# Performance work log

Measured on AMD Instinct MI355X. Metric: run time of the kernel, lower is better.

The kernel has to match this reference:

```python
import jax, jax.numpy as jnp
import numpy as np


def conv1d(x, w, b, pad):
    # x: [B,C,T], w: [O,I,K]
    y = jax.lax.conv_general_dilated(x, w, (1,), [(pad, pad)],
                                     dimension_numbers=('NCH', 'OIH', 'NCH'))
    return y + b[None, :, None]


def setup_inputs() -> dict:
    key = jax.random.key(0)
    ks = jax.random.split(key, 16)
    s = 0.05
    return {
        'x':    jax.random.normal(ks[0], (1024, 512), dtype=jnp.float32),
        'w1':   jax.random.normal(ks[1], (5, 1, 3), dtype=jnp.float32) * s,
        'b1':   jnp.zeros((5,), jnp.float32),
        'w2':   jax.random.normal(ks[2], (10, 5, 5), dtype=jnp.float32) * s,
        'b2':   jnp.zeros((10,), jnp.float32),
        'w3':   jax.random.normal(ks[3], (10, 10, 7), dtype=jnp.float32) * s,
        'b3':   jnp.zeros((10,), jnp.float32),
        'code': jax.random.uniform(ks[4], (10, 32), dtype=jnp.float32),
        'd1w':  jax.random.normal(ks[5], (10, 10, 5), dtype=jnp.float32) * s,
        'd1b':  jnp.zeros((10,), jnp.float32),
        'd2w':  jax.random.normal(ks[6], (10, 10, 5), dtype=jnp.float32) * s,
        'd2b':  jnp.zeros((10,), jnp.float32),
        'fcw':  jax.random.normal(ks[7], (512, 5120), dtype=jnp.float32) * 0.01,
        'fcb':  jnp.zeros((512,), jnp.float32),
    }


def reference(x, w1, b1, w2, b2, w3, b3, code, d1w, d1b, d2w, d2b, fcw, fcb):
    B = x.shape[0]
    h = x[:, None, :]                                   # [B,1,512]
    h = jax.nn.relu(conv1d(h, w1, b1, 1))               # [B,5,512]
    h = jax.nn.relu(conv1d(h, w2, b2, 2))               # [B,10,512]
    h = jnp.tanh(conv1d(h, w3, b3, 3))                  # [B,10,512]
    # squared distance: sum_c (h[b,c,t] - code[c,k])^2 -> [B,512,32]
    x2 = jnp.sum(h * h, axis=1)                         # [B,512]
    cross = jnp.einsum('bct,ck->btk', h, code)          # [B,512,32]
    c2 = jnp.sum(code * code, axis=0)                   # [32]
    dist = x2[:, :, None] - 2.0 * cross + c2[None, None, :]
    prob = jax.nn.softmax(-dist, axis=-1)               # [B,512,32]
    q = jnp.einsum('btk,ck->btc', prob, code)           # [B,512,10]
    h = q.transpose(0, 2, 1)                            # [B,10,512]
    h = jax.nn.relu(conv1d(h, d1w, d1b, 2))
    h = jax.nn.relu(conv1d(h, d2w, d2b, 2))
    flat = h.reshape(B, -1)                             # [B,5120]
    return jnp.tanh(flat @ fcw.T + fcb)                 # [B,512]
```

## Files before the change

### kernel.cpp

```cpp
#include <hip/hip_runtime.h>
#include <hip/hip_bf16.h>

#define TT 512
#define RS 16
#define RH 8
#define NROW 528
#define K_FC 5120

typedef _Float16 h8 __attribute__((ext_vector_type(8)));
typedef float f32x16 __attribute__((ext_vector_type(16)));
typedef __attribute__((address_space(1))) const void GAS;
typedef __attribute__((address_space(3))) void LAS;

__device__ __forceinline__ float fast_tanh(float v) {
    float e = __expf(2.0f * v);
    return 1.0f - 2.0f / (e + 1.0f);
}
__device__ __forceinline__ unsigned pk(float a, float b) {
    return __builtin_bit_cast(unsigned, __builtin_amdgcn_cvt_pkrtz(a, b));
}

__global__ __launch_bounds__(256) void prep_wtab_kernel(
    const float* __restrict__ w2, const float* __restrict__ w3,
    const float* __restrict__ d1w, const float* __restrict__ d2w,
    const float* __restrict__ code, uint4* __restrict__ wtab,
    unsigned* __restrict__ c2tab)
{
    const int i = blockIdx.x * 256 + threadIdx.x;
    if (i < 1600) {
        const int lane = i & 63;
        const int o = lane & 31;
        const int hi = lane >> 5;
        h8 v = {};
        if (i < 320) {
            const int j = i >> 6;
            #pragma unroll
            for (int e = 0; e < 8; ++e) {
                int k = hi * 8 + e;
                if (o < 10 && k < 5) v[e] = (_Float16)w2[(o * 5 + k) * 5 + j];
            }
        } else if (i < 768) {
            const int j = (i - 320) >> 6;
            #pragma unroll
            for (int e = 0; e < 8; ++e) {
                int k = hi * 8 + e;
                if (o < 10 && k < 10) v[e] = (_Float16)w3[(o * 10 + k) * 7 + j];
            }
        } else if (i < 1088) {
            const int j = (i - 768) >> 6;
            #pragma unroll
            for (int e = 0; e < 8; ++e) {
                int k = hi * 8 + e;
                if (o < 10 && k < 10) v[e] = (_Float16)d1w[(o * 10 + k) * 5 + j];
            }
        } else if (i < 1408) {
            const int j = (i - 1088) >> 6;
            #pragma unroll
            for (int e = 0; e < 8; ++e) {
                int k = hi * 8 + e;
                if (o < 10 && k < 10) v[e] = (_Float16)d2w[(o * 10 + k) * 5 + j];
            }
        } else if (i < 1472) {
            #pragma unroll
            for (int e = 0; e < 8; ++e) {
                int ch = hi * 8 + e;
                if (ch < 10) v[e] = (_Float16)(2.0f * code[ch * 32 + o]);
            }
        } else {
            const int ks = (i - 1472) >> 6;
            #pragma unroll
            for (int e = 0; e < 8; ++e) {
                int kc = ks * 16 + hi * 8 + e;
                if (o < 10) v[e] = (_Float16)code[o * 32 + kc];
            }
        }
        wtab[i] = __builtin_bit_cast(uint4, v);
    } else if (i < 1632) {
        int k = i - 1600;
        float s = 0.f;
        for (int c = 0; c < 10; ++c) { float cv = code[c * 32 + k]; s = fmaf(cv, cv, s); }
        c2tab[k] = __float_as_uint(4.0f - s);
    }
}

template<int J, int P, int ACT>
__device__ __forceinline__ void conv_stage(
    const _Float16* __restrict__ src, _Float16* __restrict__ dst,
    const uint4* __restrict__ wtab, int wbase, const float* __restrict__ bsrc)
{
    const int tid = threadIdx.x;
    const int lane = tid & 63;
    const int wv = tid >> 6;
    const int l31 = lane & 31;
    const int hi = lane >> 5;

    uint4 wf[J];
    #pragma unroll
    for (int j = 0; j < J; ++j) wf[j] = wtab[wbase + j * 64 + lane];
    float bias[6];
    #pragma unroll
    for (int r = 0; r < 6; ++r) {
        int m = (r & 3) + 8 * (r >> 2) + 4 * hi;
        bias[r] = (m < 10) ? bsrc[m] : 0.f;
    }

    #pragma unroll 2
    for (int tile = 0; tile < 4; ++tile) {
        const int tcol = wv * 128 + tile * 32 + l31;
        f32x16 acc = {};
        #pragma unroll
        for (int j = 0; j < J; ++j) {
            h8 bf = *(const h8*)(src + (tcol + RH - P + j) * RS + hi * 8);
            acc = __builtin_amdgcn_mfma_f32_32x32x16_f16(
                __builtin_bit_cast(h8, wf[j]), bf, acc, 0, 0, 0);
        }
        float v[6];
        #pragma unroll
        for (int r = 0; r < 6; ++r) {
            float t = acc[r] + bias[r];
            v[r] = (ACT == 0) ? fmaxf(t, 0.f) : fast_tanh(t);
        }
        unsigned* drow = (unsigned*)(dst + (tcol + RH) * RS);
        drow[hi * 2 + 0] = pk(v[0], v[1]);
        drow[hi * 2 + 1] = pk(v[2], v[3]);
        if (!hi) drow[4] = pk(v[4], v[5]);
    }
}

template<int J, int P>
__device__ __forceinline__ void conv_stage_flat(
    const _Float16* __restrict__ src, _Float16* __restrict__ flatrow,
    const uint4* __restrict__ wtab, int wbase, const float* __restrict__ bsrc)
{
    const int tid = threadIdx.x;
    const int lane = tid & 63;
    const int wv = tid >> 6;
    const int l31 = lane & 31;
    const int hi = lane >> 5;

    uint4 wf[J];
    #pragma unroll
    for (int j = 0; j < J; ++j) wf[j] = wtab[wbase + j * 64 + lane];
    float bias[6];
    #pragma unroll
    for (int r = 0; r < 6; ++r) {
        int m = (r & 3) + 8 * (r >> 2) + 4 * hi;
        bias[r] = (m < 10) ? bsrc[m] : 0.f;
    }

    #pragma unroll 2
    for (int tile = 0; tile < 4; ++tile) {
        const int tcol = wv * 128 + tile * 32 + l31;
        f32x16 acc = {};
        #pragma unroll
        for (int j = 0; j < J; ++j) {
            h8 bf = *(const h8*)(src + (tcol + RH - P + j) * RS + hi * 8);
            acc = __builtin_amdgcn_mfma_f32_32x32x16_f16(
                __builtin_bit_cast(h8, wf[j]), bf, acc, 0, 0, 0);
        }
        #pragma unroll
        for (int r = 0; r < 4; ++r)
            flatrow[(r + 4 * hi) * TT + tcol] = (_Float16)fmaxf(acc[r] + bias[r], 0.f);
        if (!hi) {
            flatrow[8 * TT + tcol] = (_Float16)fmaxf(acc[4] + bias[4], 0.f);
            flatrow[9 * TT + tcol] = (_Float16)fmaxf(acc[5] + bias[5], 0.f);
        }
    }
}

__device__ __forceinline__ void vq_stage(
    const _Float16* __restrict__ src, _Float16* __restrict__ dst,
    const uint4* __restrict__ wtab, const unsigned* __restrict__ c2tab)
{
    const int tid = threadIdx.x;
    const int lane = tid & 63;
    const int wv = tid >> 6;
    const int l31 = lane & 31;
    const int hi = lane >> 5;

    const h8 wcr = __builtin_bit_cast(h8, wtab[1408 + lane]);
    const h8 wq0 = __builtin_bit_cast(h8, wtab[1472 + lane]);
    const h8 wq1 = __builtin_bit_cast(h8, wtab[1536 + lane]);
    float c2s[16];
    #pragma unroll
    for (int r = 0; r < 16; ++r)
        c2s[r] = __uint_as_float(c2tab[(r & 3) + 8 * (r >> 2) + 4 * hi]);

    #pragma unroll 2
    for (int tile = 0; tile < 4; ++tile) {
        const int tcol = wv * 128 + tile * 32 + l31;
        h8 bf = *(const h8*)(src + (tcol + RH) * RS + hi * 8);
        f32x16 sacc = {};
        sacc = __builtin_amdgcn_mfma_f32_32x32x16_f16(wcr, bf, sacc, 0, 0, 0);

        float e[16], sum = 0.f;
        #pragma unroll
        for (int r = 0; r < 16; ++r) { e[r] = __expf(sacc[r] + c2s[r]); sum += e[r]; }
        float inv = 1.0f / (sum + __shfl_xor(sum, 32));

        unsigned epk[8], sopk[8];
        #pragma unroll
        for (int q = 0; q < 8; ++q) epk[q] = pk(e[2 * q], e[2 * q + 1]);
        #pragma unroll
        for (int q = 0; q < 8; ++q) sopk[q] = (unsigned)__shfl_xor((int)epk[q], 32);

        uint4 b0u, b1u;
        b0u.x = hi ? sopk[2] : epk[0]; b0u.y = hi ? sopk[3] : epk[1];
        b0u.z = hi ? epk[2] : sopk[0]; b0u.w = hi ? epk[3] : sopk[1];
        b1u.x = hi ? sopk[6] : epk[4]; b1u.y = hi ? sopk[7] : epk[5];
        b1u.z = hi ? epk[6] : sopk[4]; b1u.w = hi ? epk[7] : sopk[5];

        f32x16 qacc = {};
        qacc = __builtin_amdgcn_mfma_f32_32x32x16_f16(wq0, __builtin_bit_cast(h8, b0u), qacc, 0, 0, 0);
        qacc = __builtin_amdgcn_mfma_f32_32x32x16_f16(wq1, __builtin_bit_cast(h8, b1u), qacc, 0, 0, 0);

        float v[6];
        #pragma unroll
        for (int r = 0; r < 6; ++r) v[r] = qacc[r] * inv;
        unsigned* drow = (unsigned*)(dst + (tcol + RH) * RS);
        drow[hi * 2 + 0] = pk(v[0], v[1]);
        drow[hi * 2 + 1] = pk(v[2], v[3]);
        if (!hi) drow[4] = pk(v[4], v[5]);
    }
}

__global__ __launch_bounds__(256, 4) void enc_dec_kernel(
    const float* __restrict__ x,
    const float* __restrict__ w1, const float* __restrict__ b1,
    const float* __restrict__ b2, const float* __restrict__ b3,
    const float* __restrict__ d1b, const float* __restrict__ d2b,
    const uint4* __restrict__ wtab, const unsigned* __restrict__ c2tab,
    _Float16* __restrict__ flat,
    const float* __restrict__ fcw, _Float16* __restrict__ fcw_h, int nenc)
{
    __shared__ __align__(16) _Float16 bufA[NROW * RS];
    __shared__ __align__(16) _Float16 bufB[NROW * RS];

    const int tid = threadIdx.x;
    const int bid = blockIdx.x;

    if (bid >= nenc) {
        int i = (bid - nenc) * 256 + tid;
        float4 a = ((const float4*)fcw)[i * 2];
        float4 b4 = ((const float4*)fcw)[i * 2 + 1];
        h8 v;
        v[0] = (_Float16)a.x;  v[1] = (_Float16)a.y;
        v[2] = (_Float16)a.z;  v[3] = (_Float16)a.w;
        v[4] = (_Float16)b4.x; v[5] = (_Float16)b4.y;
        v[6] = (_Float16)b4.z; v[7] = (_Float16)b4.w;
        *(h8*)&fcw_h[(size_t)i * 8] = v;
        return;
    }

    if (tid < 32) {
        int r = tid >> 1, half = tid & 1;
        int row = (r < 8) ? r : 512 + r;
        uint4 z = {0, 0, 0, 0};
        *(uint4*)(bufA + row * RS + half * 8) = z;
    }
    {
        uint4 z = {0, 0, 0, 0};
        uint4* pb = (uint4*)bufB;
        for (int i = tid; i < NROW * RS / 8; i += 256) pb[i] = z;
    }

    {
        const float* xrow = x + (size_t)bid * TT;
        const int t0 = tid * 2;
        float xm  = (t0 > 0) ? xrow[t0 - 1] : 0.f;
        float x0v = xrow[t0];
        float x1v = xrow[t0 + 1];
        float xp  = (t0 < TT - 2) ? xrow[t0 + 2] : 0.f;
        h8 r0 = {}, r1 = {};
        #pragma unroll
        for (int o = 0; o < 5; ++o) {
            float k0 = w1[o * 3], k1 = w1[o * 3 + 1], k2 = w1[o * 3 + 2], bb = b1[o];
            float a0 = fmaf(k0, xm,  fmaf(k1, x0v, fmaf(k2, x1v, bb)));
            float a1 = fmaf(k0, x0v, fmaf(k1, x1v, fmaf(k2, xp,  bb)));
            r0[o] = (_Float16)fmaxf(a0, 0.f);
            r1[o] = (_Float16)fmaxf(a1, 0.f);
        }
        h8 zz = {};
        *(h8*)&bufA[(t0 + RH) * RS] = r0;
        *(h8*)&bufA[(t0 + RH) * RS + 8] = zz;
        *(h8*)&bufA[(t0 + 1 + RH) * RS] = r1;
        *(h8*)&bufA[(t0 + 1 + RH) * RS + 8] = zz;
    }
    __syncthreads();

    conv_stage<5, 2, 0>(bufA, bufB, wtab, 0,    b2);
    __syncthreads();
    conv_stage<7, 3, 1>(bufB, bufA, wtab, 320,  b3);
    __syncthreads();
    vq_stage(bufA, bufB, wtab, c2tab);
    __syncthreads();
    conv_stage<5, 2, 0>(bufB, bufA, wtab, 768,  d1b);
    __syncthreads();
    conv_stage_flat<5, 2>(bufA, flat + (size_t)bid * (10 * TT),
                          wtab, 1088, d2b);
}

__global__ __launch_bounds__(256, 1) void fc_mfma_kernel(
    const _Float16* __restrict__ A,
    const _Float16* __restrict__ W,
    const float* __restrict__ bias,
    float* __restrict__ out)
{
    __shared__ __align__(16) unsigned char smem[49152];

    const int tid  = threadIdx.x;
    const int lane = tid & 63;
    const int w    = tid >> 6;

    const int bid = blockIdx.x;
    const int swz = (bid & 7) * 32 + (bid >> 3);
    const int m0 = (swz >> 4) * 64;
    const int n0 = (swz & 15) * 32;

    const int l31 = lane & 31;
    const int lh  = lane >> 5;
    const int rl16 = lane >> 4;
    const int c_lds = lane & 15;

    f32x16 acc0 = {}, acc1 = {};

    const _Float16* Asrc = A + (size_t)m0 * K_FC;
    const _Float16* Wsrc = W + (size_t)n0 * K_FC;

    auto stage = [&](int buf, int s) {
        unsigned char* Ad = smem + buf * 24576;
        unsigned char* Bd = Ad + 16384;
        const int k0 = s * 128;
        #pragma unroll
        for (int j = 0; j < 4; ++j) {
            const int i = w * 4 + j;
            const int rloc = 4 * i + rl16;
            const int csrc = c_lds ^ (rloc & 7);
            __builtin_amdgcn_global_load_lds(
                (GAS*)(Asrc + (size_t)rloc * K_FC + k0 + csrc * 8),
                (LAS*)(Ad + i * 1024), 16, 0, 0);
        }
        #pragma unroll
        for (int j = 0; j < 2; ++j) {
            const int i = w * 2 + j;
            const int rloc = 4 * i + rl16;
            const int csrc = c_lds ^ (rloc & 7);
            __builtin_amdgcn_global_load_lds(
                (GAS*)(Wsrc + (size_t)rloc * K_FC + k0 + csrc * 8),
                (LAS*)(Bd + i * 1024), 16, 0, 0);
        }
    };

    stage(0, 0);
    __syncthreads();

    for (int s = 0; s < 40; ++s) {
        const int cur = s & 1;
        if (s + 1 < 40) stage(cur ^ 1, s + 1);

        const unsigned char* Ab = smem + cur * 24576;
        const unsigned char* Bb = Ab + 16384;
        #pragma unroll
        for (int ks = 0; ks < 2; ++ks) {
            const int chunk = w * 4 + ks * 2 + lh;
            const int swzo  = ((chunk ^ (lane & 7)) << 4);
            h8 af0 = *(const h8*)(Ab +        l31 * 256 + swzo);
            h8 af1 = *(const h8*)(Ab + 8192 + l31 * 256 + swzo);
            h8 bf  = *(const h8*)(Bb +        l31 * 256 + swzo);
            acc0 = __builtin_amdgcn_mfma_f32_32x32x16_f16(af0, bf, acc0, 0, 0, 0);
            acc1 = __builtin_amdgcn_mfma_f32_32x32x16_f16(af1, bf, acc1, 0, 0, 0);
        }
        __syncthreads();
    }

    float* red = (float*)smem;
    {
        float* base = red + w * 2048;
        #pragma unroll
        for (int rq = 0; rq < 4; ++rq) {
            float4 v;
            v.x = acc0[rq*4+0]; v.y = acc0[rq*4+1]; v.z = acc0[rq*4+2]; v.w = acc0[rq*4+3];
            *(float4*)&base[rq * 256 + lane * 4] = v;
            v.x = acc1[rq*4+0]; v.y = acc1[rq*4+1]; v.z = acc1[rq*4+2]; v.w = acc1[rq*4+3];
            *(float4*)&base[1024 + rq * 256 + lane * 4] = v;
        }
    }
    __syncthreads();
    {
        const int lo   = tid & 63;
        const int mf   = (tid >> 6) & 1;
        const int half = tid >> 7;
        const int n    = lo & 31;
        const float bv = bias[n0 + n];
        #pragma unroll
        for (int q = 0; q < 2; ++q) {
            const int rq = half * 2 + q;
            const int idx = mf * 1024 + rq * 256 + lo * 4;
            float4 s0 = *(const float4*)&red[idx];
            float4 s1 = *(const float4*)&red[2048 + idx];
            float4 s2 = *(const float4*)&red[4096 + idx];
            float4 s3 = *(const float4*)&red[6144 + idx];
            #pragma unroll
            for (int rr = 0; rr < 4; ++rr) {
                float sum = ((const float*)&s0)[rr] + ((const float*)&s1)[rr]
                          + ((const float*)&s2)[rr] + ((const float*)&s3)[rr];
                const int m = mf * 32 + rr + 8 * rq + 4 * (lo >> 5);
                out[(size_t)(m0 + m) * 512 + n0 + n] = fast_tanh(sum + bv);
            }
        }
    }
}

extern "C" void kernel_launch(void* const* d_in, const int* in_sizes, int n_in,
                              void* d_out, int out_size, void* d_ws, size_t ws_size,
                              hipStream_t stream) {
    const float* x    = (const float*)d_in[0];
    const float* w1   = (const float*)d_in[1];
    const float* b1   = (const float*)d_in[2];
    const float* w2   = (const float*)d_in[3];
    const float* b2   = (const float*)d_in[4];
    const float* w3   = (const float*)d_in[5];
    const float* b3   = (const float*)d_in[6];
    const float* code = (const float*)d_in[7];
    const float* d1w  = (const float*)d_in[8];
    const float* d1b  = (const float*)d_in[9];
    const float* d2w  = (const float*)d_in[10];
    const float* d2b  = (const float*)d_in[11];
    const float* fcw  = (const float*)d_in[12];
    const float* fcb  = (const float*)d_in[13];
    float* out = (float*)d_out;

    _Float16* flat_h = (_Float16*)d_ws;
    _Float16* fcw_h  = (_Float16*)((char*)d_ws + 10485760);
    uint4*    wtab   = (uint4*)((char*)d_ws + 15728640);
    unsigned* c2tab  = (unsigned*)((char*)d_ws + 15728640 + 25600);

    const int Bsz = in_sizes[0] / TT;

    prep_wtab_kernel<<<7, 256, 0, stream>>>(w2, w3, d1w, d2w, code, wtab, c2tab);
    enc_dec_kernel<<<Bsz + 1280, 256, 0, stream>>>(x, w1, b1, b2, b3, d1b, d2b,
                                                   wtab, c2tab, flat_h,
                                                   fcw, fcw_h, Bsz);
    fc_mfma_kernel<<<256, 256, 0, stream>>>(flat_h, fcw_h, fcb, out);
}
```

Measured before the change: 55.24 us.

## Fuse conv3 with VQ stage in registers and interleave fcw conversion blocks

```diff
diff --git a/kernel.cpp b/kernel.cpp
--- a/kernel.cpp
+++ b/kernel.cpp
@@ -18,6 +18,9 @@
 }
 __device__ __forceinline__ unsigned pk(float a, float b) {
     return __builtin_bit_cast(unsigned, __builtin_amdgcn_cvt_pkrtz(a, b));
+}
+__device__ __forceinline__ unsigned sx32(unsigned v) {
+    return (unsigned)__shfl_xor((int)v, 32);
 }
 
 __global__ __launch_bounds__(256) void prep_wtab_kernel(
@@ -121,8 +124,8 @@
             v[r] = (ACT == 0) ? fmaxf(t, 0.f) : fast_tanh(t);
         }
         unsigned* drow = (unsigned*)(dst + (tcol + RH) * RS);
-        drow[hi * 2 + 0] = pk(v[0], v[1]);
-        drow[hi * 2 + 1] = pk(v[2], v[3]);
+        uint2 s1v; s1v.x = pk(v[0], v[1]); s1v.y = pk(v[2], v[3]);
+        *(uint2*)(drow + hi * 2) = s1v;
         if (!hi) drow[4] = pk(v[4], v[5]);
     }
 }
@@ -168,9 +171,10 @@
     }
 }
 
-__device__ __forceinline__ void vq_stage(
+__device__ __forceinline__ void conv3_vq_stage(
     const _Float16* __restrict__ src, _Float16* __restrict__ dst,
-    const uint4* __restrict__ wtab, const unsigned* __restrict__ c2tab)
+    const uint4* __restrict__ wtab, const float* __restrict__ bsrc,
+    const unsigned* __restrict__ c2tab)
 {
     const int tid = threadIdx.x;
     const int lane = tid & 63;
@@ -178,20 +182,48 @@
     const int l31 = lane & 31;
     const int hi = lane >> 5;
 
+    uint4 wf[7];
+    #pragma unroll
+    for (int j = 0; j < 7; ++j) wf[j] = wtab[320 + j * 64 + lane];
     const h8 wcr = __builtin_bit_cast(h8, wtab[1408 + lane]);
     const h8 wq0 = __builtin_bit_cast(h8, wtab[1472 + lane]);
     const h8 wq1 = __builtin_bit_cast(h8, wtab[1536 + lane]);
+    float bias[6];
+    #pragma unroll
+    for (int r = 0; r < 6; ++r) {
+        int m = (r & 3) + 8 * (r >> 2) + 4 * hi;
+        bias[r] = (m < 10) ? bsrc[m] : 0.f;
+    }
     float c2s[16];
     #pragma unroll
     for (int r = 0; r < 16; ++r)
         c2s[r] = __uint_as_float(c2tab[(r & 3) + 8 * (r >> 2) + 4 * hi]);
 
-    #pragma unroll 2
+    #pragma unroll 1
     for (int tile = 0; tile < 4; ++tile) {
         const int tcol = wv * 128 + tile * 32 + l31;
-        h8 bf = *(const h8*)(src + (tcol + RH) * RS + hi * 8);
+        f32x16 acc = {};
+        #pragma unroll
+        for (int j = 0; j < 7; ++j) {
+            h8 bf = *(const h8*)(src + (tcol + RH - 3 + j) * RS + hi * 8);
+            acc = __builtin_amdgcn_mfma_f32_32x32x16_f16(
+                __builtin_bit_cast(h8, wf[j]), bf, acc, 0, 0, 0);
+        }
+        float v[6];
+        #pragma unroll
+        for (int r = 0; r < 6; ++r) v[r] = fast_tanh(acc[r] + bias[r]);
+
+        unsigned p01 = pk(v[0], v[1]), p23 = pk(v[2], v[3]), p45 = pk(v[4], v[5]);
+        unsigned o01 = sx32(p01), o23 = sx32(p23), o45 = sx32(p45);
+        uint4 bu;
+        bu.x = hi ? o45 : p01;
+        bu.y = hi ? 0u  : p23;
+        bu.z = hi ? 0u  : o01;
+        bu.w = hi ? 0u  : o23;
+
         f32x16 sacc = {};
-        sacc = __builtin_amdgcn_mfma_f32_32x32x16_f16(wcr, bf, sacc, 0, 0, 0);
+        sacc = __builtin_amdgcn_mfma_f32_32x32x16_f16(
+            wcr, __builtin_bit_cast(h8, bu), sacc, 0, 0, 0);
 
         float e[16], sum = 0.f;
         #pragma unroll
@@ -202,7 +234,7 @@
         #pragma unroll
         for (int q = 0; q < 8; ++q) epk[q] = pk(e[2 * q], e[2 * q + 1]);
         #pragma unroll
-        for (int q = 0; q < 8; ++q) sopk[q] = (unsigned)__shfl_xor((int)epk[q], 32);
+        for (int q = 0; q < 8; ++q) sopk[q] = sx32(epk[q]);
 
         uint4 b0u, b1u;
         b0u.x = hi ? sopk[2] : epk[0]; b0u.y = hi ? sopk[3] : epk[1];
@@ -214,13 +246,13 @@
         qacc = __builtin_amdgcn_mfma_f32_32x32x16_f16(wq0, __builtin_bit_cast(h8, b0u), qacc, 0, 0, 0);
         qacc = __builtin_amdgcn_mfma_f32_32x32x16_f16(wq1, __builtin_bit_cast(h8, b1u), qacc, 0, 0, 0);
 
-        float v[6];
-        #pragma unroll
-        for (int r = 0; r < 6; ++r) v[r] = qacc[r] * inv;
+        float q6[6];
+        #pragma unroll
+        for (int r = 0; r < 6; ++r) q6[r] = qacc[r] * inv;
         unsigned* drow = (unsigned*)(dst + (tcol + RH) * RS);
-        drow[hi * 2 + 0] = pk(v[0], v[1]);
-        drow[hi * 2 + 1] = pk(v[2], v[3]);
-        if (!hi) drow[4] = pk(v[4], v[5]);
+        uint2 s1v; s1v.x = pk(q6[0], q6[1]); s1v.y = pk(q6[2], q6[3]);
+        *(uint2*)(drow + hi * 2) = s1v;
+        if (!hi) drow[4] = pk(q6[4], q6[5]);
     }
 }
 
@@ -239,8 +271,16 @@
     const int tid = threadIdx.x;
     const int bid = blockIdx.x;
 
-    if (bid >= nenc) {
-        int i = (bid - nenc) * 256 + tid;
+    int row = 0, cvt = -1;
+    if (nenc == 1024) {
+        const int g = bid / 9, r = bid % 9;
+        if (r < 4) row = g * 4 + r; else cvt = g * 5 + (r - 4);
+    } else {
+        if (bid >= nenc) cvt = bid - nenc; else row = bid;
+    }
+
+    if (cvt >= 0) {
+        int i = cvt * 256 + tid;
         float4 a = ((const float4*)fcw)[i * 2];
         float4 b4 = ((const float4*)fcw)[i * 2 + 1];
         h8 v;
@@ -254,9 +294,9 @@
 
     if (tid < 32) {
         int r = tid >> 1, half = tid & 1;
-        int row = (r < 8) ? r : 512 + r;
+        int rowz = (r < 8) ? r : 512 + r;
         uint4 z = {0, 0, 0, 0};
-        *(uint4*)(bufA + row * RS + half * 8) = z;
+        *(uint4*)(bufA + rowz * RS + half * 8) = z;
     }
     {
         uint4 z = {0, 0, 0, 0};
@@ -265,7 +305,7 @@
     }
 
     {
-        const float* xrow = x + (size_t)bid * TT;
+        const float* xrow = x + (size_t)row * TT;
         const int t0 = tid * 2;
         float xm  = (t0 > 0) ? xrow[t0 - 1] : 0.f;
         float x0v = xrow[t0];
@@ -288,15 +328,13 @@
     }
     __syncthreads();
 
-    conv_stage<5, 2, 0>(bufA, bufB, wtab, 0,    b2);
-    __syncthreads();
-    conv_stage<7, 3, 1>(bufB, bufA, wtab, 320,  b3);
-    __syncthreads();
-    vq_stage(bufA, bufB, wtab, c2tab);
-    __syncthreads();
-    conv_stage<5, 2, 0>(bufB, bufA, wtab, 768,  d1b);
-    __syncthreads();
-    conv_stage_flat<5, 2>(bufA, flat + (size_t)bid * (10 * TT),
+    conv_stage<5, 2, 0>(bufA, bufB, wtab, 0, b2);
+    __syncthreads();
+    conv3_vq_stage(bufB, bufA, wtab, b3, c2tab);
+    __syncthreads();
+    conv_stage<5, 2, 0>(bufA, bufB, wtab, 768, d1b);
+    __syncthreads();
+    conv_stage_flat<5, 2>(bufB, flat + (size_t)row * (10 * TT),
                           wtab, 1088, d2b);
 }
 
```

Result: slower. 57.19 us (+3.5%).

## Split FC GEMM into split-K partial tiles with separate reduce kernel

Applied to the files above, without the earlier changes.

```diff
diff --git a/kernel.cpp b/kernel.cpp
--- a/kernel.cpp
+++ b/kernel.cpp
@@ -121,8 +121,8 @@
             v[r] = (ACT == 0) ? fmaxf(t, 0.f) : fast_tanh(t);
         }
         unsigned* drow = (unsigned*)(dst + (tcol + RH) * RS);
-        drow[hi * 2 + 0] = pk(v[0], v[1]);
-        drow[hi * 2 + 1] = pk(v[2], v[3]);
+        uint2 s1v; s1v.x = pk(v[0], v[1]); s1v.y = pk(v[2], v[3]);
+        *(uint2*)(drow + hi * 2) = s1v;
         if (!hi) drow[4] = pk(v[4], v[5]);
     }
 }
@@ -218,8 +218,8 @@
         #pragma unroll
         for (int r = 0; r < 6; ++r) v[r] = qacc[r] * inv;
         unsigned* drow = (unsigned*)(dst + (tcol + RH) * RS);
-        drow[hi * 2 + 0] = pk(v[0], v[1]);
-        drow[hi * 2 + 1] = pk(v[2], v[3]);
+        uint2 s1v; s1v.x = pk(v[0], v[1]); s1v.y = pk(v[2], v[3]);
+        *(uint2*)(drow + hi * 2) = s1v;
         if (!hi) drow[4] = pk(v[4], v[5]);
     }
 }
@@ -254,9 +254,9 @@
 
     if (tid < 32) {
         int r = tid >> 1, half = tid & 1;
-        int row = (r < 8) ? r : 512 + r;
+        int rowz = (r < 8) ? r : 512 + r;
         uint4 z = {0, 0, 0, 0};
-        *(uint4*)(bufA + row * RS + half * 8) = z;
+        *(uint4*)(bufA + rowz * RS + half * 8) = z;
     }
     {
         uint4 z = {0, 0, 0, 0};
@@ -288,127 +288,116 @@
     }
     __syncthreads();
 
-    conv_stage<5, 2, 0>(bufA, bufB, wtab, 0,    b2);
-    __syncthreads();
-    conv_stage<7, 3, 1>(bufB, bufA, wtab, 320,  b3);
+    conv_stage<5, 2, 0>(bufA, bufB, wtab, 0, b2);
+    __syncthreads();
+    conv_stage<7, 3, 1>(bufB, bufA, wtab, 320, b3);
     __syncthreads();
     vq_stage(bufA, bufB, wtab, c2tab);
     __syncthreads();
-    conv_stage<5, 2, 0>(bufB, bufA, wtab, 768,  d1b);
+    conv_stage<5, 2, 0>(bufB, bufA, wtab, 768, d1b);
     __syncthreads();
     conv_stage_flat<5, 2>(bufA, flat + (size_t)bid * (10 * TT),
                           wtab, 1088, d2b);
 }
 
-__global__ __launch_bounds__(256, 1) void fc_mfma_kernel(
+__global__ __launch_bounds__(256, 1) void fc_partial_kernel(
     const _Float16* __restrict__ A,
     const _Float16* __restrict__ W,
-    const float* __restrict__ bias,
-    float* __restrict__ out)
+    float* __restrict__ partial)
 {
     __shared__ __align__(16) unsigned char smem[49152];
 
-    const int tid  = threadIdx.x;
+    const int tid = threadIdx.x;
     const int lane = tid & 63;
-    const int w    = tid >> 6;
+    const int w = tid >> 6;
+    const int l31 = lane & 31;
+    const int hi = lane >> 5;
 
     const int bid = blockIdx.x;
-    const int swz = (bid & 7) * 32 + (bid >> 3);
-    const int m0 = (swz >> 4) * 64;
-    const int n0 = (swz & 15) * 32;
-
-    const int l31 = lane & 31;
-    const int lh  = lane >> 5;
-    const int rl16 = lane >> 4;
-    const int c_lds = lane & 15;
+    const int tile = (bid & 7) | ((bid >> 5) << 3);
+    const int ks4  = (bid >> 3) & 3;
+    const int m0 = (tile >> 3) * 128;
+    const int n0 = (tile & 7) * 64;
+    const int kbase = ks4 * 1280;
+
+    const _Float16* Asrc = A + (size_t)m0 * K_FC + kbase;
+    const _Float16* Wsrc = W + (size_t)n0 * K_FC + kbase;
 
     f32x16 acc0 = {}, acc1 = {};
-
-    const _Float16* Asrc = A + (size_t)m0 * K_FC;
-    const _Float16* Wsrc = W + (size_t)n0 * K_FC;
 
     auto stage = [&](int buf, int s) {
         unsigned char* Ad = smem + buf * 24576;
         unsigned char* Bd = Ad + 16384;
-        const int k0 = s * 128;
-        #pragma unroll
-        for (int j = 0; j < 4; ++j) {
-            const int i = w * 4 + j;
-            const int rloc = 4 * i + rl16;
-            const int csrc = c_lds ^ (rloc & 7);
+        const int k0 = s * 64;
+        #pragma unroll
+        for (int p = 0; p < 4; ++p) {
+            const int idx = p * 256 + tid;
+            const int row = idx >> 3;
+            const int c = idx & 7;
+            const int csrc = c ^ (row & 7);
             __builtin_amdgcn_global_load_lds(
-                (GAS*)(Asrc + (size_t)rloc * K_FC + k0 + csrc * 8),
-                (LAS*)(Ad + i * 1024), 16, 0, 0);
-        }
-        #pragma unroll
-        for (int j = 0; j < 2; ++j) {
-            const int i = w * 2 + j;
-            const int rloc = 4 * i + rl16;
-            const int csrc = c_lds ^ (rloc & 7);
+                (GAS*)(Asrc + (size_t)row * K_FC + k0 + csrc * 8),
+                (LAS*)(Ad + idx * 16), 16, 0, 0);
+        }
+        #pragma unroll
+        for (int p = 0; p < 2; ++p) {
+            const int idx = p * 256 + tid;
+            const int row = idx >> 3;
+            const int c = idx & 7;
+            const int csrc = c ^ (row & 7);
             __builtin_amdgcn_global_load_lds(
-                (GAS*)(Wsrc + (size_t)rloc * K_FC + k0 + csrc * 8),
-                (LAS*)(Bd + i * 1024), 16, 0, 0);
+                (GAS*)(Wsrc + (size_t)row * K_FC + k0 + csrc * 8),
+                (LAS*)(Bd + idx * 16), 16, 0, 0);
         }
     };
 
     stage(0, 0);
     __syncthreads();
 
-    for (int s = 0; s < 40; ++s) {
+    for (int s = 0; s < 20; ++s) {
         const int cur = s & 1;
-        if (s + 1 < 40) stage(cur ^ 1, s + 1);
+        if (s + 1 < 20) stage(cur ^ 1, s + 1);
 
         const unsigned char* Ab = smem + cur * 24576;
         const unsigned char* Bb = Ab + 16384;
-        #pragma unroll
-        for (int ks = 0; ks < 2; ++ks) {
-            const int chunk = w * 4 + ks * 2 + lh;
-            const int swzo  = ((chunk ^ (lane & 7)) << 4);
-            h8 af0 = *(const h8*)(Ab +        l31 * 256 + swzo);
-            h8 af1 = *(const h8*)(Ab + 8192 + l31 * 256 + swzo);
-            h8 bf  = *(const h8*)(Bb +        l31 * 256 + swzo);
-            acc0 = __builtin_amdgcn_mfma_f32_32x32x16_f16(af0, bf, acc0, 0, 0, 0);
-            acc1 = __builtin_amdgcn_mfma_f32_32x32x16_f16(af1, bf, acc1, 0, 0, 0);
+        const int ar = w * 32 + l31;
+        #pragma unroll
+        for (int ks = 0; ks < 4; ++ks) {
+            const int kc = ks * 2 + hi;
+            h8 af  = *(const h8*)(Ab + ar * 128 + ((kc ^ (ar & 7)) << 4));
+            h8 bf0 = *(const h8*)(Bb + l31 * 128 + ((kc ^ (l31 & 7)) << 4));
+            h8 bf1 = *(const h8*)(Bb + (l31 + 32) * 128 + ((kc ^ ((l31 + 32) & 7)) << 4));
+            acc0 = __builtin_amdgcn_mfma_f32_32x32x16_f16(af, bf0, acc0, 0, 0, 0);
+            acc1 = __builtin_amdgcn_mfma_f32_32x32x16_f16(af, bf1, acc1, 0, 0, 0);
         }
         __syncthreads();
     }
 
-    float* red = (float*)smem;
-    {
-        float* base = red + w * 2048;
-        #pragma unroll
-        for (int rq = 0; rq < 4; ++rq) {
-            float4 v;
-            v.x = acc0[rq*4+0]; v.y = acc0[rq*4+1]; v.z = acc0[rq*4+2]; v.w = acc0[rq*4+3];
-            *(float4*)&base[rq * 256 + lane * 4] = v;
-            v.x = acc1[rq*4+0]; v.y = acc1[rq*4+1]; v.z = acc1[rq*4+2]; v.w = acc1[rq*4+3];
-            *(float4*)&base[1024 + rq * 256 + lane * 4] = v;
-        }
-    }
-    __syncthreads();
-    {
-        const int lo   = tid & 63;
-        const int mf   = (tid >> 6) & 1;
-        const int half = tid >> 7;
-        const int n    = lo & 31;
-        const float bv = bias[n0 + n];
-        #pragma unroll
-        for (int q = 0; q < 2; ++q) {
-            const int rq = half * 2 + q;
-            const int idx = mf * 1024 + rq * 256 + lo * 4;
-            float4 s0 = *(const float4*)&red[idx];
-            float4 s1 = *(const float4*)&red[2048 + idx];
-            float4 s2 = *(const float4*)&red[4096 + idx];
-            float4 s3 = *(const float4*)&red[6144 + idx];
-            #pragma unroll
-            for (int rr = 0; rr < 4; ++rr) {
-                float sum = ((const float*)&s0)[rr] + ((const float*)&s1)[rr]
-                          + ((const float*)&s2)[rr] + ((const float*)&s3)[rr];
-                const int m = mf * 32 + rr + 8 * rq + 4 * (lo >> 5);
-                out[(size_t)(m0 + m) * 512 + n0 + n] = fast_tanh(sum + bv);
-            }
-        }
-    }
+    float* base = partial + (size_t)ks4 * (1024 * 512);
+    #pragma unroll
+    for (int r = 0; r < 16; ++r) {
+        const int m = m0 + w * 32 + (r & 3) + 8 * (r >> 2) + 4 * hi;
+        base[(size_t)m * 512 + n0 + l31]      = acc0[r];
+        base[(size_t)m * 512 + n0 + 32 + l31] = acc1[r];
+    }
+}
+
+__global__ __launch_bounds__(256) void fc_reduce_kernel(
+    const float* __restrict__ partial, const float* __restrict__ bias,
+    float* __restrict__ out)
+{
+    const int i = (blockIdx.x * 256 + threadIdx.x) * 2;
+    float2 p0 = *(const float2*)&partial[i];
+    float2 p1 = *(const float2*)&partial[524288 + i];
+    float2 p2 = *(const float2*)&partial[1048576 + i];
+    float2 p3 = *(const float2*)&partial[1572864 + i];
+    const int n = i & 511;
+    float s0 = p0.x + p1.x + p2.x + p3.x + bias[n];
+    float s1 = p0.y + p1.y + p2.y + p3.y + bias[n + 1];
+    float2 o;
+    o.x = fast_tanh(s0);
+    o.y = fast_tanh(s1);
+    *(float2*)&out[i] = o;
 }
 
 extern "C" void kernel_launch(void* const* d_in, const int* in_sizes, int n_in,
@@ -430,10 +419,11 @@
     const float* fcb  = (const float*)d_in[13];
     float* out = (float*)d_out;
 
-    _Float16* flat_h = (_Float16*)d_ws;
-    _Float16* fcw_h  = (_Float16*)((char*)d_ws + 10485760);
-    uint4*    wtab   = (uint4*)((char*)d_ws + 15728640);
-    unsigned* c2tab  = (unsigned*)((char*)d_ws + 15728640 + 25600);
+    _Float16* flat_h  = (_Float16*)d_ws;
+    _Float16* fcw_h   = (_Float16*)((char*)d_ws + 10485760);
+    float*    partial = (float*)((char*)d_ws + 16777216);
+    uint4*    wtab    = (uint4*)((char*)d_ws + 25165824);
+    unsigned* c2tab   = (unsigned*)((char*)d_ws + 25165824 + 25600);
 
     const int Bsz = in_sizes[0] / TT;
 
@@ -441,5 +431,6 @@
     enc_dec_kernel<<<Bsz + 1280, 256, 0, stream>>>(x, w1, b1, b2, b3, d1b, d2b,
                                                    wtab, c2tab, flat_h,
                                                    fcw, fcw_h, Bsz);
-    fc_mfma_kernel<<<256, 256, 0, stream>>>(flat_h, fcw_h, fcb, out);
-}
+    fc_partial_kernel<<<256, 256, 0, stream>>>(flat_h, fcw_h, partial);
+    fc_reduce_kernel<<<1024, 256, 0, stream>>>(partial, fcb, out);
+}
```

New measurement: 47.69 us. -13.7%, faster.
